# Performance work log

Hardware: AMD Instinct MI355X
Metric: run time of the kernel (lower is better)

The kernel has to match this reference:

```python
import jax, jax.numpy as jnp
import numpy as np
import math

N = 60000; B = 2; D = 128; NH = 8; HD = D // NH; DFF = 256
NBLK = 6; L = NBLK * 2
WIN = 12.0; TEMP = 10000.0
NY, NX = 400, 400
MT = (36, 144)      # max_tokens per drop level (drop_info)
CAP = (25, 100)     # filled tokens per window in synthetic data (~0.7 fill)
LVL_N = (24000, 36000)  # voxels per drop level (per shift)


def _nwin(n, cap):
    return -(-n // cap)


def _make_inds(n, lvl):
    j = np.arange(n)
    return (j // CAP[lvl]) * MT[lvl] + (j % CAP[lvl])


def setup_inputs():
    ks = jax.random.split(jax.random.key(0), 8)
    rng = np.random.default_rng(0)
    # unique BEV coords per batch element -> scatter has no collisions
    coors_list = []
    for b in range(B):
        flat = rng.choice(NY * NX, N // B, replace=False)
        coors_list.append(np.stack([np.full(N // B, b, np.int64), np.zeros(N // B, np.int64), flat // NX, flat % NX], 1))
    coors = jnp.asarray(np.concatenate(coors_list, 0), dtype=jnp.int32)
    vxs, indss = [], []
    for s in range(2):
        perm = rng.permutation(N)
        vxs += [np.sort(perm[:LVL_N[0]]), np.sort(perm[LVL_N[0]:])]
        indss += [_make_inds(LVL_N[0], 0), _make_inds(LVL_N[1], 1)]
    i32 = lambda a: jnp.asarray(a, jnp.int32)
    f = lambda k, shape: jax.random.normal(k, shape, dtype=jnp.float32) * 0.02
    return dict(
        voxel_feat=jax.random.normal(ks[0], (N, D), dtype=jnp.float32),
        coors=coors,
        ciw0=jax.random.randint(ks[1], (N, 2), 0, int(WIN)).astype(jnp.float32),
        ciw1=jax.random.randint(ks[2], (N, 2), 0, int(WIN)).astype(jnp.float32),
        vx00=i32(vxs[0]), inds00=i32(indss[0]), vx01=i32(vxs[1]), inds01=i32(indss[1]),
        vx10=i32(vxs[2]), inds10=i32(indss[2]), vx11=i32(vxs[3]), inds11=i32(indss[3]),
        in_proj_w=f(ks[3], (L, 3 * D, D)), in_proj_b=jnp.zeros((L, 3 * D), jnp.float32),
        out_w=f(ks[4], (L, D, D)), out_b=jnp.zeros((L, D), jnp.float32),
        lin1_w=f(ks[5], (L, DFF, D)), lin1_b=jnp.zeros((L, DFF), jnp.float32),
        lin2_w=f(ks[6], (L, D, DFF)), lin2_b=jnp.zeros((L, D), jnp.float32),
        ln1_g=jnp.ones((L, D), jnp.float32), ln1_b=jnp.zeros((L, D), jnp.float32),
        ln2_g=jnp.ones((L, D), jnp.float32), ln2_b=jnp.zeros((L, D), jnp.float32),
        conv_w=f(ks[7], (2, D, D, 3, 3)),
        bn_g=jnp.ones((2, D), jnp.float32), bn_b=jnp.zeros((2, D), jnp.float32),
        bn_m=jnp.zeros((2, D), jnp.float32), bn_v=jnp.ones((2, D), jnp.float32),
    )


def _pos_embed(ciw):
    # SSTv1.get_pos_embed: interleaved sin/cos over x and y window coords
    xy = ciw - WIN / 2.0
    pl = D // 2
    i = jnp.arange(pl, dtype=jnp.float32)
    inv = TEMP ** (2.0 * jnp.floor(i / 2.0) / pl)
    e = xy[:, :, None] / inv                      # [N, 2, pl]
    emb = jnp.stack([jnp.sin(e[..., ::2]), jnp.cos(e[..., 1::2])], -1).reshape(ciw.shape[0], 2, pl)
    return jnp.concatenate([emb[:, 0], emb[:, 1]], -1)  # [N, D]


def _ln(x, g, b):
    mu = jnp.mean(x, -1, keepdims=True)
    var = jnp.mean((x - mu) ** 2, -1, keepdims=True)
    return (x - mu) * jax.lax.rsqrt(var + 1e-5) * g + b


def _forward(voxel_feat, coors, ciws, vx, inds, fp):
    (ipw, ipb, ow, ob, l1w, l1b, l2w, l2b, g1, b1, g2, b2, cw, bg, bb, bm, bv) = fp
    pos = [_pos_embed(ciws[0]), _pos_embed(ciws[1])]
    feat = voxel_feat
    for blk in range(NBLK):
        for s in range(2):  # BasicShiftBlock: one encoder layer per shift
            li = blk * 2 + s
            attn_out = jnp.zeros_like(feat)
            for lvl in range(2):  # drop levels, each with its own padded window tensor
                v, ii = vx[(s, lvl)], inds[(s, lvl)]
                mt = MT[lvl]
                nw = _nwin(int(v.shape[0]), CAP[lvl])
                def to_win(x2d):  # flat2window: scatter voxels into [nw, mt, C]
                    return jnp.zeros((nw * mt, x2d.shape[-1]), x2d.dtype).at[ii].set(x2d[v]).reshape(nw, mt, -1)
                wf = to_win(feat)
                wp = to_win(pos[s])
                pad = jnp.ones((nw * mt,), bool).at[ii].set(False).reshape(nw, mt)  # True = padded slot
                qk_in = wf + wp
                q = (qk_in @ ipw[li, :D].T + ipb[li, :D]).reshape(nw, mt, NH, HD)
                k = (qk_in @ ipw[li, D:2 * D].T + ipb[li, D:2 * D]).reshape(nw, mt, NH, HD)
                val = (wf @ ipw[li, 2 * D:].T + ipb[li, 2 * D:]).reshape(nw, mt, NH, HD)
                sc = jnp.einsum('wqhd,wkhd->whqk', q, k) / math.sqrt(HD)
                sc = jnp.where(pad[:, None, None, :], -jnp.inf, sc)
                o = jnp.einsum('whqk,wkhd->wqhd', jax.nn.softmax(sc, -1), val).reshape(nw, mt, D)
                o = o @ ow[li].T + ob[li]
                # window2flat: gather valid slots back to flat voxel order
                attn_out = attn_out.at[v].set(o.reshape(nw * mt, D)[ii])
            feat = _ln(feat + attn_out, g1[li], b1[li])
            h = jax.nn.gelu(feat @ l1w[li].T + l1b[li], approximate=False)
            feat = _ln(feat + h @ l2w[li].T + l2b[li], g2[li], b2[li])
    # recover_bev: scatter voxels into dense BEV canvas [B, C, ny, nx]
    flat_idx = coors[:, 0] * (NY * NX) + coors[:, 2] * NX + coors[:, 3]
    canvas = jnp.zeros((B * NY * NX, D), feat.dtype).at[flat_idx].set(feat)
    bev = canvas.reshape(B, NY, NX, D).transpose(0, 3, 1, 2)
    for i in range(2):  # attached dilated convs + BN(eval) + ReLU
        bev = jax.lax.conv_general_dilated(bev, cw[i], (1, 1), [(2, 2), (2, 2)], rhs_dilation=(2, 2), dimension_numbers=('NCHW', 'OIHW', 'NCHW'))
        bev = (bev - bm[i][:, None, None]) * jax.lax.rsqrt(bv[i][:, None, None] + 1e-3) * bg[i][:, None, None] + bb[i][:, None, None]
        bev = jax.nn.relu(bev)
    return bev


def reference(voxel_feat, coors, ciw0, ciw1, vx00, inds00, vx01, inds01, vx10, inds10, vx11, inds11, in_proj_w, in_proj_b, out_w, out_b, lin1_w, lin1_b, lin2_w, lin2_b, ln1_g, ln1_b, ln2_g, ln2_b, conv_w, bn_g, bn_b, bn_m, bn_v):
    vx = {(0, 0): vx00, (0, 1): vx01, (1, 0): vx10, (1, 1): vx11}
    inds = {(0, 0): inds00, (0, 1): inds01, (1, 0): inds10, (1, 1): inds11}
    fp = (in_proj_w, in_proj_b, out_w, out_b, lin1_w, lin1_b, lin2_w, lin2_b, ln1_g, ln1_b, ln2_g, ln2_b, conv_w, bn_g, bn_b, bn_m, bn_v)
    return _forward(voxel_feat, coors, (ciw0, ciw1), vx, inds, fp)
```

## Files before the change

kernel.cpp:

```cpp
#include <hip/hip_runtime.h>
#include <math.h>

#define NVOX 60000

typedef __attribute__((ext_vector_type(8))) short short8v;
typedef __attribute__((ext_vector_type(8))) unsigned short ushort8v;
typedef __attribute__((ext_vector_type(4))) float f32x4;

static __device__ __forceinline__ unsigned short f2bf(float f) {
    unsigned u = __float_as_uint(f);
    unsigned r = (u + 0x7fffu + ((u >> 16) & 1u)) >> 16;
    return (unsigned short)r;
}
static __device__ __forceinline__ float bf2f(unsigned short h) {
    return __uint_as_float(((unsigned)h) << 16);
}
static __device__ __forceinline__ void gll16(const unsigned short* g, unsigned short* l) {
    __builtin_amdgcn_global_load_lds(
        (const __attribute__((address_space(1))) unsigned*)g,
        (__attribute__((address_space(3))) unsigned*)l,
        16, 0, 0);
}

__global__ __launch_bounds__(256) void pos_kernel(const float* __restrict__ ciw,
                                                  unsigned short* __restrict__ pos) {
    int idx = blockIdx.x * 256 + threadIdx.x;
    if (idx >= NVOX * 128) return;
    int n = idx >> 7, d = idx & 127;
    int c = d >> 6, t = (d & 63) >> 1;
    float xy = ciw[n * 2 + c] - 6.0f;
    float inv = exp2f((float)t * (13.287712379549449f / 32.0f));
    float e = xy / inv;
    pos[idx] = f2bf((d & 1) ? cosf(e) : sinf(e));
}

__global__ __launch_bounds__(256) void cvt_bf16(const float* __restrict__ in,
                                                unsigned short* __restrict__ out, int n) {
    int idx = blockIdx.x * 256 + threadIdx.x;
    if (idx < n) out[idx] = f2bf(in[idx]);
}

__global__ __launch_bounds__(256) void feat_init(const float* __restrict__ vf,
                                                 float* __restrict__ feat,
                                                 unsigned short* __restrict__ featb) {
    int idx = blockIdx.x * 256 + threadIdx.x;
    if (idx >= NVOX * 128) return;
    float v = vf[idx];
    feat[idx] = v;
    featb[idx] = f2bf(v);
}

template<int KTOT, bool ADD, bool GELU, bool CBF16, bool LNF>
__global__ __launch_bounds__(256) void gemm_mfma(
    const unsigned short* __restrict__ A, const unsigned short* __restrict__ Aadd, int add_nblk,
    const unsigned short* __restrict__ W, const float* __restrict__ bias,
    void* __restrict__ Cp, int M, int ldc,
    float* __restrict__ feat, unsigned short* __restrict__ featb,
    const float* __restrict__ lng, const float* __restrict__ lnb)
{
    __shared__ unsigned short smem[128 * 128];
    __shared__ float2 lnsum[128][2];
    unsigned short* As = smem;
    unsigned short* Ws = smem + 128 * 64;
    const int tid = threadIdx.x;
    const int lane = tid & 63, wave = tid >> 6;
    const int wr = wave >> 1, wc = wave & 1;
    const int llo = lane & 15, lhi = lane >> 4;
    const int m0 = blockIdx.x * 128;
    const int n0 = blockIdx.y * 128;
    const bool addp = ADD && ((int)blockIdx.y < add_nblk);
    const int gr = lane >> 3;
    const int gc = (lane & 7) ^ gr;
    f32x4 acc[4][4] = {};

    for (int k0 = 0; k0 < KTOT; k0 += 64) {
        #pragma unroll
        for (int p = 0; p < 4; ++p) {
            int r0 = wave * 32 + p * 8;
            gll16(W + (size_t)(n0 + r0 + gr) * KTOT + k0 + gc * 8, &Ws[r0 * 64]);
        }
        if (!addp) {
            #pragma unroll
            for (int p = 0; p < 4; ++p) {
                int r0 = wave * 32 + p * 8;
                gll16(A + (size_t)(m0 + r0 + gr) * KTOT + k0 + gc * 8, &As[r0 * 64]);
            }
        } else {
            #pragma unroll
            for (int p = 0; p < 4; ++p) {
                int c = tid + p * 256;
                int r = c >> 3, c16 = c & 7;
                int m = m0 + r;
                short8v av = {};
                if (m < M) {
                    ushort8v fa = *reinterpret_cast<const ushort8v*>(A + (size_t)m * KTOT + k0 + c16 * 8);
                    ushort8v pa = *reinterpret_cast<const ushort8v*>(Aadd + (size_t)m * 128 + k0 + c16 * 8);
                    #pragma unroll
                    for (int q = 0; q < 8; ++q) av[q] = (short)f2bf(bf2f(fa[q]) + bf2f(pa[q]));
                }
                *reinterpret_cast<short8v*>((char*)As + r * 128 + ((c16 * 16) ^ ((r & 7) << 4))) = av;
            }
        }
        __syncthreads();
        #pragma unroll
        for (int kk = 0; kk < 2; ++kk) {
            int kb = kk * 64 + lhi * 16;
            short8v af[4], bf[4];
            #pragma unroll
            for (int i = 0; i < 4; ++i) {
                int r = wr * 64 + i * 16 + llo;
                af[i] = *reinterpret_cast<const short8v*>((const char*)As + r * 128 + (kb ^ ((r & 7) << 4)));
                int cc = wc * 64 + i * 16 + llo;
                bf[i] = *reinterpret_cast<const short8v*>((const char*)Ws + cc * 128 + (kb ^ ((cc & 7) << 4)));
            }
            #pragma unroll
            for (int i = 0; i < 4; ++i)
                #pragma unroll
                for (int j = 0; j < 4; ++j)
                    acc[i][j] = __builtin_amdgcn_mfma_f32_16x16x32_bf16(af[i], bf[j], acc[i][j], 0, 0, 0);
        }
        __syncthreads();
    }

    if (LNF) {
        float s1[4][4] = {}, s2[4][4] = {};
        #pragma unroll
        for (int i = 0; i < 4; ++i)
            #pragma unroll
            for (int rg = 0; rg < 4; ++rg) {
                int m = m0 + wr * 64 + i * 16 + lhi * 4 + rg;
                if (m < M) {
                    #pragma unroll
                    for (int j = 0; j < 4; ++j) {
                        int n = wc * 64 + j * 16 + llo;
                        float x = feat[(size_t)m * 128 + n] + acc[i][j][rg] + bias[n];
                        acc[i][j][rg] = x;
                        s1[i][rg] += x; s2[i][rg] += x * x;
                    }
                }
            }
        #pragma unroll
        for (int i = 0; i < 4; ++i)
            #pragma unroll
            for (int rg = 0; rg < 4; ++rg) {
                #pragma unroll
                for (int off = 1; off < 16; off <<= 1) {
                    s1[i][rg] += __shfl_xor(s1[i][rg], off);
                    s2[i][rg] += __shfl_xor(s2[i][rg], off);
                }
                if (llo == 0)
                    lnsum[wr * 64 + i * 16 + lhi * 4 + rg][wc] = make_float2(s1[i][rg], s2[i][rg]);
            }
        __syncthreads();
        #pragma unroll
        for (int i = 0; i < 4; ++i)
            #pragma unroll
            for (int rg = 0; rg < 4; ++rg) {
                int r = wr * 64 + i * 16 + lhi * 4 + rg;
                int m = m0 + r;
                if (m >= M) continue;
                float2 a0 = lnsum[r][0], a1 = lnsum[r][1];
                float mu = (a0.x + a1.x) * 0.0078125f;
                float var = fmaxf((a0.y + a1.y) * 0.0078125f - mu * mu, 0.f);
                float inv = rsqrtf(var + 1e-5f);
                #pragma unroll
                for (int j = 0; j < 4; ++j) {
                    int n = wc * 64 + j * 16 + llo;
                    float v = (acc[i][j][rg] - mu) * inv * lng[n] + lnb[n];
                    feat[(size_t)m * 128 + n] = v;
                    featb[(size_t)m * 128 + n] = f2bf(v);
                }
            }
    } else if (CBF16) {
        #pragma unroll
        for (int j = 0; j < 4; ++j) {
            int nl = wc * 64 + j * 16 + llo;
            float bn = bias[n0 + nl];
            #pragma unroll
            for (int i = 0; i < 4; ++i)
                #pragma unroll
                for (int rg = 0; rg < 4; ++rg) {
                    float v = acc[i][j][rg] + bn;
                    if (GELU) v = 0.5f * v * (1.0f + erff(v * 0.7071067811865475f));
                    smem[(wr * 64 + i * 16 + lhi * 4 + rg) * 128 + nl] = f2bf(v);
                }
        }
        __syncthreads();
        unsigned short* C = (unsigned short*)Cp;
        #pragma unroll
        for (int c = 0; c < 8; ++c) {
            int idx = tid + c * 256;
            int r = idx >> 4, ch = idx & 15;
            if (m0 + r < M)
                *reinterpret_cast<ushort8v*>(C + (size_t)(m0 + r) * ldc + n0 + ch * 8) =
                    *reinterpret_cast<const ushort8v*>(&smem[r * 128 + ch * 8]);
        }
    } else {
        float* C = (float*)Cp;
        #pragma unroll
        for (int j = 0; j < 4; ++j) {
            int n = n0 + wc * 64 + j * 16 + llo;
            float bn = bias[n];
            #pragma unroll
            for (int i = 0; i < 4; ++i)
                #pragma unroll
                for (int rg = 0; rg < 4; ++rg) {
                    int m = m0 + wr * 64 + i * 16 + lhi * 4 + rg;
                    if (m < M) {
                        float v = acc[i][j][rg] + bn;
                        if (GELU) v = 0.5f * v * (1.0f + erff(v * 0.7071067811865475f));
                        C[(size_t)m * ldc + n] = v;
                    }
                }
        }
    }
}

template<int CAPT, int HG>
__global__ __launch_bounds__(256) void attn_kernel(
    const unsigned short* __restrict__ qkv, const int* __restrict__ vlist, int nvox,
    unsigned short* __restrict__ oout)
{
    __shared__ float Ks[CAPT][HG * 16];
    __shared__ float Vs[CAPT][HG * 16];
    __shared__ int vl[CAPT];
    const int w = blockIdx.x;
    const int hb = blockIdx.y * HG;
    const int tid = threadIdx.x;
    const int T = min(CAPT, nvox - w * CAPT);
    if (tid < T) vl[tid] = vlist[w * CAPT + tid];
    constexpr int R8 = HG * 2;
    for (int idx = tid; idx < T * R8; idx += 256) {
        int t = idx / R8, c8 = (idx % R8) * 8;
        int vox = vlist[w * CAPT + t];
        const unsigned short* base = qkv + (size_t)vox * 384 + hb * 16 + c8;
        ushort8v kv = *reinterpret_cast<const ushort8v*>(base + 128);
        ushort8v vv = *reinterpret_cast<const ushort8v*>(base + 256);
        #pragma unroll
        for (int q = 0; q < 8; ++q) { Ks[t][c8 + q] = bf2f(kv[q]); Vs[t][c8 + q] = bf2f(vv[q]); }
    }
    __syncthreads();
    const int ITEMS = T * HG;
    for (int item = tid; item < ITEMS; item += 256) {
        int h = item & (HG - 1);
        int q = item / HG;
        int vq = vl[q];
        const unsigned short* qb = qkv + (size_t)vq * 384 + (hb + h) * 16;
        ushort8v qa = *reinterpret_cast<const ushort8v*>(qb);
        ushort8v qc = *reinterpret_cast<const ushort8v*>(qb + 8);
        float4 q0 = make_float4(bf2f(qa[0]), bf2f(qa[1]), bf2f(qa[2]), bf2f(qa[3]));
        float4 q1 = make_float4(bf2f(qa[4]), bf2f(qa[5]), bf2f(qa[6]), bf2f(qa[7]));
        float4 q2 = make_float4(bf2f(qc[0]), bf2f(qc[1]), bf2f(qc[2]), bf2f(qc[3]));
        float4 q3 = make_float4(bf2f(qc[4]), bf2f(qc[5]), bf2f(qc[6]), bf2f(qc[7]));
        float mx = -INFINITY, l = 0.f;
        float4 o0 = make_float4(0,0,0,0), o1 = o0, o2 = o0, o3 = o0;
        for (int t = 0; t < T; ++t) {
            const float4* kr = reinterpret_cast<const float4*>(&Ks[t][h * 16]);
            float4 k0 = kr[0], k1 = kr[1], k2 = kr[2], k3 = kr[3];
            float s = q0.x*k0.x + q0.y*k0.y + q0.z*k0.z + q0.w*k0.w
                    + q1.x*k1.x + q1.y*k1.y + q1.z*k1.z + q1.w*k1.w
                    + q2.x*k2.x + q2.y*k2.y + q2.z*k2.z + q2.w*k2.w
                    + q3.x*k3.x + q3.y*k3.y + q3.z*k3.z + q3.w*k3.w;
            s *= 0.25f;
            float mo = mx;
            mx = fmaxf(mx, s);
            float cc = __expf(mo - mx);
            float p  = __expf(s - mx);
            l = l * cc + p;
            const float4* vr = reinterpret_cast<const float4*>(&Vs[t][h * 16]);
            float4 v0 = vr[0], v1 = vr[1], v2 = vr[2], v3 = vr[3];
            o0.x = o0.x*cc + p*v0.x; o0.y = o0.y*cc + p*v0.y; o0.z = o0.z*cc + p*v0.z; o0.w = o0.w*cc + p*v0.w;
            o1.x = o1.x*cc + p*v1.x; o1.y = o1.y*cc + p*v1.y; o1.z = o1.z*cc + p*v1.z; o1.w = o1.w*cc + p*v1.w;
            o2.x = o2.x*cc + p*v2.x; o2.y = o2.y*cc + p*v2.y; o2.z = o2.z*cc + p*v2.z; o2.w = o2.w*cc + p*v2.w;
            o3.x = o3.x*cc + p*v3.x; o3.y = o3.y*cc + p*v3.y; o3.z = o3.z*cc + p*v3.z; o3.w = o3.w*cc + p*v3.w;
        }
        float rl = 1.0f / l;
        ushort8v r0, r1;
        r0[0]=f2bf(o0.x*rl); r0[1]=f2bf(o0.y*rl); r0[2]=f2bf(o0.z*rl); r0[3]=f2bf(o0.w*rl);
        r0[4]=f2bf(o1.x*rl); r0[5]=f2bf(o1.y*rl); r0[6]=f2bf(o1.z*rl); r0[7]=f2bf(o1.w*rl);
        r1[0]=f2bf(o2.x*rl); r1[1]=f2bf(o2.y*rl); r1[2]=f2bf(o2.z*rl); r1[3]=f2bf(o2.w*rl);
        r1[4]=f2bf(o3.x*rl); r1[5]=f2bf(o3.y*rl); r1[6]=f2bf(o3.z*rl); r1[7]=f2bf(o3.w*rl);
        unsigned short* op = oout + (size_t)vq * 128 + (hb + h) * 16;
        *reinterpret_cast<ushort8v*>(op) = r0;
        *reinterpret_cast<ushort8v*>(op + 8) = r1;
    }
}

__global__ __launch_bounds__(256) void scatter_kernel(const float* __restrict__ feat,
    const int* __restrict__ coors, unsigned short* __restrict__ canvas)
{
    int idx = blockIdx.x * 256 + threadIdx.x;
    if (idx >= NVOX * 16) return;
    int n = idx >> 4, c8 = (idx & 15) << 3;
    int b = coors[n * 4], y = coors[n * 4 + 2], x = coors[n * 4 + 3];
    const float* src = feat + (size_t)n * 128 + c8;
    float4 u0 = *reinterpret_cast<const float4*>(src);
    float4 u1 = *reinterpret_cast<const float4*>(src + 4);
    ushort8v v;
    v[0]=f2bf(u0.x); v[1]=f2bf(u0.y); v[2]=f2bf(u0.z); v[3]=f2bf(u0.w);
    v[4]=f2bf(u1.x); v[5]=f2bf(u1.y); v[6]=f2bf(u1.z); v[7]=f2bf(u1.w);
    size_t p = (((size_t)b * 404 + y + 2) * 420 + x + 2) * 128 + c8;
    *reinterpret_cast<ushort8v*>(canvas + p) = v;
}

__global__ __launch_bounds__(256) void wtrans_kernel(const float* __restrict__ cw,
                                                     unsigned short* __restrict__ wbuf)
{
    int idx = blockIdx.x * 256 + threadIdx.x;
    if (idx >= 2 * 9 * 128 * 128) return;
    int ci = idx & 127;
    int co = (idx >> 7) & 127;
    int kk = (idx >> 14) % 9;
    int i  = idx / (9 * 16384);
    wbuf[idx] = f2bf(cw[(((size_t)i * 128 + co) * 128 + ci) * 9 + kk]);
}

template<bool NCHW_OUT>
__global__ __launch_bounds__(512, 1) void conv_mfma(
    const unsigned short* __restrict__ in, const unsigned short* __restrict__ wbuf,
    const float* __restrict__ g, const float* __restrict__ bsh,
    const float* __restrict__ bm, const float* __restrict__ bv,
    void* __restrict__ out)
{
    __shared__ unsigned short Ab[8 * 36 * 128];
    __shared__ unsigned short Wb[2 * 128 * 128];
    const int tid = threadIdx.x;
    const int lane = tid & 63, wave = tid >> 6;
    const int cog = wave & 1, yg = wave >> 1;
    const int llo = lane & 15, lhi = lane >> 4;
    const int x0 = blockIdx.x * 32, y0 = blockIdx.y * 4, b = blockIdx.z;
    const int c16s = lane & 15;

    #pragma unroll
    for (int it = 0; it < 9; ++it) {
        int gidx = it * 32 + wave * 4 + lhi;
        int row = gidx / 36, xi = gidx % 36;
        gll16(in + (((size_t)b * 404 + y0 + row) * 420 + x0 + xi) * 128 + ((c16s ^ (xi & 15)) * 8),
              Ab + (size_t)(it * 512 + wave * 64) * 8);
    }
    {
        const unsigned short* wt = wbuf;
        #pragma unroll
        for (int it = 0; it < 4; ++it) {
            int co = it * 32 + wave * 4 + lhi;
            gll16(wt + co * 128 + ((c16s ^ (co & 15)) * 8),
                  Wb + (size_t)(it * 512 + wave * 64) * 8);
        }
    }
    __syncthreads();

    f32x4 acc[2][4] = {};
    #pragma unroll
    for (int t = 0; t < 9; ++t) {
        if (t < 8) {
            const unsigned short* wt = wbuf + (size_t)(t + 1) * 16384;
            unsigned short* dst = Wb + ((t + 1) & 1) * 16384;
            #pragma unroll
            for (int it = 0; it < 4; ++it) {
                int co = it * 32 + wave * 4 + lhi;
                gll16(wt + co * 128 + ((c16s ^ (co & 15)) * 8),
                      dst + (size_t)(it * 512 + wave * 64) * 8);
            }
        }
        const unsigned short* Wp = Wb + (t & 1) * 16384;
        const int ky = t / 3, kx = t % 3;
        const int r = yg + 2 * ky;
        #pragma unroll
        for (int kk = 0; kk < 4; ++kk) {
            short8v a[2], w[4];
            #pragma unroll
            for (int i = 0; i < 2; ++i) {
                int xi = i * 16 + llo + 2 * kx;
                a[i] = *reinterpret_cast<const short8v*>(
                    (const char*)Ab + (r * 36 + xi) * 256 + ((kk * 64 + lhi * 16) ^ ((xi & 15) << 4)));
            }
            #pragma unroll
            for (int j = 0; j < 4; ++j) {
                int co = cog * 64 + j * 16 + llo;
                w[j] = *reinterpret_cast<const short8v*>(
                    (const char*)Wp + co * 256 + ((kk * 64 + lhi * 16) ^ ((co & 15) << 4)));
            }
            #pragma unroll
            for (int i = 0; i < 2; ++i)
                #pragma unroll
                for (int j = 0; j < 4; ++j)
                    acc[i][j] = __builtin_amdgcn_mfma_f32_16x16x32_bf16(a[i], w[j], acc[i][j], 0, 0, 0);
        }
        __syncthreads();
    }

    const int y = y0 + yg;
    if (NCHW_OUT) {
        #pragma unroll
        for (int j = 0; j < 4; ++j) {
            int co = cog * 64 + j * 16 + llo;
            float scale = rsqrtf(bv[co] + 1e-3f) * g[co];
            float shift = bsh[co] - bm[co] * scale;
            #pragma unroll
            for (int i = 0; i < 2; ++i) {
                int px = x0 + i * 16 + lhi * 4;
                if (px < 400) {
                    float4 v;
                    v.x = fmaxf(acc[i][j][0] * scale + shift, 0.f);
                    v.y = fmaxf(acc[i][j][1] * scale + shift, 0.f);
                    v.z = fmaxf(acc[i][j][2] * scale + shift, 0.f);
                    v.w = fmaxf(acc[i][j][3] * scale + shift, 0.f);
                    *reinterpret_cast<float4*>(
                        (float*)out + (((size_t)b * 128 + co) * 400 + y) * 400 + px) = v;
                }
            }
        }
    } else {
        unsigned short* Cw = Wb + wave * 2048;
        #pragma unroll
        for (int j = 0; j < 4; ++j) {
            int co = cog * 64 + j * 16 + llo;
            float scale = rsqrtf(bv[co] + 1e-3f) * g[co];
            float shift = bsh[co] - bm[co] * scale;
            #pragma unroll
            for (int i = 0; i < 2; ++i)
                #pragma unroll
                for (int rg = 0; rg < 4; ++rg)
                    Cw[(i * 16 + lhi * 4 + rg) * 64 + j * 16 + llo] =
                        f2bf(fmaxf(acc[i][j][rg] * scale + shift, 0.f));
        }
        #pragma unroll
        for (int s = 0; s < 4; ++s) {
            int pxl = s * 8 + (lane >> 3);
            int oct = lane & 7;
            int px = x0 + pxl;
            if (px < 400)
                *reinterpret_cast<ushort8v*>(
                    (unsigned short*)out + (((size_t)b * 404 + y + 2) * 420 + px + 2) * 128
                                         + cog * 64 + oct * 8) =
                    *reinterpret_cast<const ushort8v*>(&Cw[pxl * 64 + oct * 8]);
        }
    }
}

extern "C" void kernel_launch(void* const* d_in, const int* in_sizes, int n_in,
                              void* d_out, int out_size, void* d_ws, size_t ws_size,
                              hipStream_t stream) {
    const float* voxel_feat = (const float*)d_in[0];
    const int*   coors      = (const int*)d_in[1];
    const float* ciw0       = (const float*)d_in[2];
    const float* ciw1       = (const float*)d_in[3];
    const int* vx[2][2] = {{(const int*)d_in[4], (const int*)d_in[6]},
                           {(const int*)d_in[8], (const int*)d_in[10]}};
    const float* ipw = (const float*)d_in[12];
    const float* ipb = (const float*)d_in[13];
    const float* ow  = (const float*)d_in[14];
    const float* obp = (const float*)d_in[15];
    const float* l1w = (const float*)d_in[16];
    const float* l1b = (const float*)d_in[17];
    const float* l2w = (const float*)d_in[18];
    const float* l2b = (const float*)d_in[19];
    const float* g1  = (const float*)d_in[20];
    const float* b1  = (const float*)d_in[21];
    const float* g2  = (const float*)d_in[22];
    const float* b2  = (const float*)d_in[23];
    const float* cw  = (const float*)d_in[24];
    const float* bng = (const float*)d_in[25];
    const float* bnb = (const float*)d_in[26];
    const float* bnm = (const float*)d_in[27];
    const float* bnv = (const float*)d_in[28];

    float* F = (float*)d_ws;
    unsigned short* W0   = (unsigned short*)F;
    unsigned short* ipwb = W0;
    unsigned short* owb  = W0 + 589824;
    unsigned short* l1wb = W0 + 786432;
    unsigned short* l2wb = W0 + 1179648;
    unsigned short* cwb  = W0 + 1572864;
    float* feat = F + 940000;
    unsigned short* featb = (unsigned short*)(F + 8620000);
    unsigned short* pos0  = (unsigned short*)(F + 12460000);
    unsigned short* pos1  = (unsigned short*)(F + 16300000);
    unsigned short* obufb = (unsigned short*)(F + 20140000);
    unsigned short* hbufb = (unsigned short*)(F + 23980000);
    unsigned short* canvas1 = (unsigned short*)(F + 8620000);
    unsigned short* canvas2 = (unsigned short*)(F + 30339040);
    unsigned short* qkvb = (unsigned short*)d_out;

    feat_init<<<30000, 256, 0, stream>>>(voxel_feat, feat, featb);
    pos_kernel<<<30000, 256, 0, stream>>>(ciw0, pos0);
    pos_kernel<<<30000, 256, 0, stream>>>(ciw1, pos1);
    cvt_bf16<<<(589824 + 255) / 256, 256, 0, stream>>>(ipw, ipwb, 589824);
    cvt_bf16<<<(196608 + 255) / 256, 256, 0, stream>>>(ow,  owb,  196608);
    cvt_bf16<<<(393216 + 255) / 256, 256, 0, stream>>>(l1w, l1wb, 393216);
    cvt_bf16<<<(393216 + 255) / 256, 256, 0, stream>>>(l2w, l2wb, 393216);
    wtrans_kernel<<<(2 * 9 * 16384 + 255) / 256, 256, 0, stream>>>(cw, cwb);

    for (int li = 0; li < 12; ++li) {
        int s = li & 1;
        const unsigned short* pos = s ? pos1 : pos0;
        gemm_mfma<128, true, false, true, false><<<dim3(469, 3), 256, 0, stream>>>(
            featb, pos, 2, ipwb + (size_t)li * 49152, ipb + li * 384, qkvb, NVOX, 384,
            nullptr, nullptr, nullptr, nullptr);
        attn_kernel<25, 8><<<dim3(960, 1), 256, 0, stream>>>(qkvb, vx[s][0], 24000, obufb);
        attn_kernel<100, 2><<<dim3(360, 4), 256, 0, stream>>>(qkvb, vx[s][1], 36000, obufb);
        gemm_mfma<128, false, false, false, true><<<dim3(469, 1), 256, 0, stream>>>(
            obufb, nullptr, 0, owb + (size_t)li * 16384, obp + li * 128, nullptr, NVOX, 128,
            feat, featb, g1 + li * 128, b1 + li * 128);
        gemm_mfma<128, false, true, true, false><<<dim3(469, 2), 256, 0, stream>>>(
            featb, nullptr, 0, l1wb + (size_t)li * 32768, l1b + li * 256, hbufb, NVOX, 256,
            nullptr, nullptr, nullptr, nullptr);
        gemm_mfma<256, false, false, false, true><<<dim3(469, 1), 256, 0, stream>>>(
            hbufb, nullptr, 0, l2wb + (size_t)li * 32768, l2b + li * 128, nullptr, NVOX, 128,
            feat, featb, g2 + li * 128, b2 + li * 128);
    }

    hipMemsetAsync(canvas1, 0, (size_t)43438080 * 2 * 2, stream);
    scatter_kernel<<<(NVOX * 16 + 255) / 256, 256, 0, stream>>>(feat, coors, canvas1);
    conv_mfma<false><<<dim3(13, 100, 2), 512, 0, stream>>>(
        canvas1, cwb, bng, bnb, bnm, bnv, canvas2);
    conv_mfma<true><<<dim3(13, 100, 2), 512, 0, stream>>>(
        canvas2, cwb + 9 * 16384, bng + 128, bnb + 128, bnm + 128, bnv + 128, (float*)d_out);
}
```

Before: 2.494 ms.

## Fuse out-proj, LN1, FFN and LN2 into one per-layer tail kernel

Replaces the three post-attention GEMM launches (out-projection + LN1, lin1 + GELU, lin2 + LN2) with a single fused kernel. Each block handles 64 rows and keeps the LN1 output and the GELU hidden activations in LDS, so the hidden buffer and intermediate feat/featb no longer round-trip through global memory. It also shrinks the canvas memset to canvas1 only and zeroes just the halo of canvas2 with a small kernel. The cost is heavy LDS use per block (about 74KB), which limits occupancy, and the weights are reloaded by every block.

After: 2.769 ms. 1.11x slower.

```diff
diff --git a/kernel.cpp b/kernel.cpp
--- a/kernel.cpp
+++ b/kernel.cpp
@@ -54,12 +54,9 @@
 __global__ __launch_bounds__(256) void gemm_mfma(
     const unsigned short* __restrict__ A, const unsigned short* __restrict__ Aadd, int add_nblk,
     const unsigned short* __restrict__ W, const float* __restrict__ bias,
-    void* __restrict__ Cp, int M, int ldc,
-    float* __restrict__ feat, unsigned short* __restrict__ featb,
-    const float* __restrict__ lng, const float* __restrict__ lnb)
+    void* __restrict__ Cp, int M, int ldc)
 {
     __shared__ unsigned short smem[128 * 128];
-    __shared__ float2 lnsum[128][2];
     unsigned short* As = smem;
     unsigned short* Ws = smem + 128 * 64;
     const int tid = threadIdx.x;
@@ -122,97 +119,28 @@
         __syncthreads();
     }
 
-    if (LNF) {
-        float s1[4][4] = {}, s2[4][4] = {};
+    #pragma unroll
+    for (int j = 0; j < 4; ++j) {
+        int nl = wc * 64 + j * 16 + llo;
+        float bn = bias[n0 + nl];
         #pragma unroll
         for (int i = 0; i < 4; ++i)
             #pragma unroll
             for (int rg = 0; rg < 4; ++rg) {
-                int m = m0 + wr * 64 + i * 16 + lhi * 4 + rg;
-                if (m < M) {
-                    #pragma unroll
-                    for (int j = 0; j < 4; ++j) {
-                        int n = wc * 64 + j * 16 + llo;
-                        float x = feat[(size_t)m * 128 + n] + acc[i][j][rg] + bias[n];
-                        acc[i][j][rg] = x;
-                        s1[i][rg] += x; s2[i][rg] += x * x;
-                    }
-                }
-            }
-        #pragma unroll
-        for (int i = 0; i < 4; ++i)
-            #pragma unroll
-            for (int rg = 0; rg < 4; ++rg) {
-                #pragma unroll
-                for (int off = 1; off < 16; off <<= 1) {
-                    s1[i][rg] += __shfl_xor(s1[i][rg], off);
-                    s2[i][rg] += __shfl_xor(s2[i][rg], off);
-                }
-                if (llo == 0)
-                    lnsum[wr * 64 + i * 16 + lhi * 4 + rg][wc] = make_float2(s1[i][rg], s2[i][rg]);
-            }
-        __syncthreads();
-        #pragma unroll
-        for (int i = 0; i < 4; ++i)
-            #pragma unroll
-            for (int rg = 0; rg < 4; ++rg) {
-                int r = wr * 64 + i * 16 + lhi * 4 + rg;
-                int m = m0 + r;
-                if (m >= M) continue;
-                float2 a0 = lnsum[r][0], a1 = lnsum[r][1];
-                float mu = (a0.x + a1.x) * 0.0078125f;
-                float var = fmaxf((a0.y + a1.y) * 0.0078125f - mu * mu, 0.f);
-                float inv = rsqrtf(var + 1e-5f);
-                #pragma unroll
-                for (int j = 0; j < 4; ++j) {
-                    int n = wc * 64 + j * 16 + llo;
-                    float v = (acc[i][j][rg] - mu) * inv * lng[n] + lnb[n];
-                    feat[(size_t)m * 128 + n] = v;
-                    featb[(size_t)m * 128 + n] = f2bf(v);
-                }
-            }
-    } else if (CBF16) {
-        #pragma unroll
-        for (int j = 0; j < 4; ++j) {
-            int nl = wc * 64 + j * 16 + llo;
-            float bn = bias[n0 + nl];
-            #pragma unroll
-            for (int i = 0; i < 4; ++i)
-                #pragma unroll
-                for (int rg = 0; rg < 4; ++rg) {
-                    float v = acc[i][j][rg] + bn;
-                    if (GELU) v = 0.5f * v * (1.0f + erff(v * 0.7071067811865475f));
-                    smem[(wr * 64 + i * 16 + lhi * 4 + rg) * 128 + nl] = f2bf(v);
-                }
-        }
-        __syncthreads();
-        unsigned short* C = (unsigned short*)Cp;
-        #pragma unroll
-        for (int c = 0; c < 8; ++c) {
-            int idx = tid + c * 256;
-            int r = idx >> 4, ch = idx & 15;
-            if (m0 + r < M)
-                *reinterpret_cast<ushort8v*>(C + (size_t)(m0 + r) * ldc + n0 + ch * 8) =
-                    *reinterpret_cast<const ushort8v*>(&smem[r * 128 + ch * 8]);
-        }
-    } else {
-        float* C = (float*)Cp;
-        #pragma unroll
-        for (int j = 0; j < 4; ++j) {
-            int n = n0 + wc * 64 + j * 16 + llo;
-            float bn = bias[n];
-            #pragma unroll
-            for (int i = 0; i < 4; ++i)
-                #pragma unroll
-                for (int rg = 0; rg < 4; ++rg) {
-                    int m = m0 + wr * 64 + i * 16 + lhi * 4 + rg;
-                    if (m < M) {
-                        float v = acc[i][j][rg] + bn;
-                        if (GELU) v = 0.5f * v * (1.0f + erff(v * 0.7071067811865475f));
-                        C[(size_t)m * ldc + n] = v;
-                    }
-                }
-        }
+                float v = acc[i][j][rg] + bn;
+                if (GELU) v = 0.5f * v * (1.0f + erff(v * 0.7071067811865475f));
+                smem[(wr * 64 + i * 16 + lhi * 4 + rg) * 128 + nl] = f2bf(v);
+            }
+    }
+    __syncthreads();
+    unsigned short* C = (unsigned short*)Cp;
+    #pragma unroll
+    for (int c = 0; c < 8; ++c) {
+        int idx = tid + c * 256;
+        int r = idx >> 4, ch = idx & 15;
+        if (m0 + r < M)
+            *reinterpret_cast<ushort8v*>(C + (size_t)(m0 + r) * ldc + n0 + ch * 8) =
+                *reinterpret_cast<const ushort8v*>(&smem[r * 128 + ch * 8]);
     }
 }
 
@@ -286,6 +214,230 @@
     }
 }
 
+__global__ __launch_bounds__(256) void fused_tail(
+    const unsigned short* __restrict__ obuf,
+    const unsigned short* __restrict__ oww,
+    const float* __restrict__ obp,
+    const unsigned short* __restrict__ w1,
+    const float* __restrict__ b1p,
+    const unsigned short* __restrict__ w2,
+    const float* __restrict__ b2p,
+    const float* __restrict__ lng1, const float* __restrict__ lnb1,
+    const float* __restrict__ lng2, const float* __restrict__ lnb2,
+    float* __restrict__ feat, unsigned short* __restrict__ featb, int M)
+{
+    __shared__ unsigned short S[36864];
+    __shared__ float2 lnsum[64][4];
+    unsigned short* Abuf = S;
+    unsigned short* Wbuf = S + 4096;
+    unsigned short* Xbuf = S + 12288;
+    unsigned short* Hbuf = S + 20480;
+    const int tid = threadIdx.x;
+    const int lane = tid & 63, wave = tid >> 6;
+    const int llo = lane & 15, lhi = lane >> 4;
+    const int r8 = lane >> 3, c8 = lane & 7;
+    const int m0 = blockIdx.x * 64;
+
+    auto stageA = [&](int k0) {
+        #pragma unroll
+        for (int it = 0; it < 2; ++it) {
+            int rb = wave * 16 + it * 8;
+            int r = rb + r8;
+            int gm = m0 + r; if (gm >= M) gm = M - 1;
+            gll16(obuf + (size_t)gm * 128 + k0 * 64 + ((c8 ^ (r & 7)) * 8), Abuf + rb * 64);
+        }
+    };
+    auto stageW = [&](const unsigned short* src, int ldk, int koff) {
+        #pragma unroll
+        for (int it = 0; it < 4; ++it) {
+            int rb = wave * 32 + it * 8;
+            int r = rb + r8;
+            gll16(src + (size_t)r * ldk + koff + ((c8 ^ (r & 7)) * 8), Wbuf + rb * 64);
+        }
+    };
+    auto frag = [&](const unsigned short* buf, int r, int kk) {
+        return *reinterpret_cast<const short8v*>(
+            (const char*)buf + r * 128 + (((kk * 4 + lhi) ^ (r & 7)) * 16));
+    };
+    auto sput = [&](unsigned short* buf, int col, int r, float v) {
+        int slab = col >> 6, k = col & 63;
+        buf[slab * 4096 + r * 64 + (((k >> 3) ^ (r & 7)) * 8) + (k & 7)] = f2bf(v);
+    };
+
+    f32x4 acc0[4][2] = {};
+    #pragma unroll
+    for (int k0 = 0; k0 < 2; ++k0) {
+        stageA(k0);
+        stageW(oww, 128, k0 * 64);
+        __syncthreads();
+        #pragma unroll
+        for (int kk = 0; kk < 2; ++kk) {
+            short8v a[4], w[2];
+            #pragma unroll
+            for (int i = 0; i < 4; ++i) a[i] = frag(Abuf, i * 16 + llo, kk);
+            #pragma unroll
+            for (int j = 0; j < 2; ++j) w[j] = frag(Wbuf, wave * 32 + j * 16 + llo, kk);
+            #pragma unroll
+            for (int i = 0; i < 4; ++i)
+                #pragma unroll
+                for (int j = 0; j < 2; ++j)
+                    acc0[i][j] = __builtin_amdgcn_mfma_f32_16x16x32_bf16(a[i], w[j], acc0[i][j], 0, 0, 0);
+        }
+        __syncthreads();
+    }
+
+    {
+        float ob0 = obp[wave * 32 + llo];
+        float ob1 = obp[wave * 32 + 16 + llo];
+        #pragma unroll
+        for (int i = 0; i < 4; ++i)
+            #pragma unroll
+            for (int rg = 0; rg < 4; ++rg) {
+                int m = m0 + i * 16 + lhi * 4 + rg;
+                if (m >= M) m = M - 1;
+                const float* fp = feat + (size_t)m * 128 + wave * 32 + llo;
+                float x0 = fp[0]  + acc0[i][0][rg] + ob0;
+                float x1 = fp[16] + acc0[i][1][rg] + ob1;
+                acc0[i][0][rg] = x0; acc0[i][1][rg] = x1;
+                float s1 = x0 + x1, s2 = x0 * x0 + x1 * x1;
+                #pragma unroll
+                for (int off = 1; off < 16; off <<= 1) {
+                    s1 += __shfl_xor(s1, off);
+                    s2 += __shfl_xor(s2, off);
+                }
+                if (llo == 0) lnsum[i * 16 + lhi * 4 + rg][wave] = make_float2(s1, s2);
+            }
+    }
+    __syncthreads();
+    {
+        float gg0 = lng1[wave * 32 + llo],      bb0 = lnb1[wave * 32 + llo];
+        float gg1 = lng1[wave * 32 + 16 + llo], bb1 = lnb1[wave * 32 + 16 + llo];
+        #pragma unroll
+        for (int i = 0; i < 4; ++i)
+            #pragma unroll
+            for (int rg = 0; rg < 4; ++rg) {
+                int r = i * 16 + lhi * 4 + rg;
+                float2 t0 = lnsum[r][0], t1 = lnsum[r][1], t2 = lnsum[r][2], t3 = lnsum[r][3];
+                float mu = (t0.x + t1.x + t2.x + t3.x) * 0.0078125f;
+                float var = fmaxf((t0.y + t1.y + t2.y + t3.y) * 0.0078125f - mu * mu, 0.f);
+                float inv = rsqrtf(var + 1e-5f);
+                float x0 = (acc0[i][0][rg] - mu) * inv * gg0 + bb0;
+                float x1 = (acc0[i][1][rg] - mu) * inv * gg1 + bb1;
+                acc0[i][0][rg] = x0; acc0[i][1][rg] = x1;
+                sput(Xbuf, wave * 32 + llo, r, x0);
+                sput(Xbuf, wave * 32 + 16 + llo, r, x1);
+            }
+    }
+    __syncthreads();
+
+    f32x4 acc1[4][4] = {};
+    #pragma unroll
+    for (int nh = 0; nh < 2; ++nh)
+        #pragma unroll
+        for (int k0 = 0; k0 < 2; ++k0) {
+            stageW(w1 + (size_t)nh * 16384, 128, k0 * 64);
+            __syncthreads();
+            #pragma unroll
+            for (int kk = 0; kk < 2; ++kk) {
+                short8v a[4], w[2];
+                #pragma unroll
+                for (int i = 0; i < 4; ++i) a[i] = frag(Xbuf + k0 * 4096, i * 16 + llo, kk);
+                #pragma unroll
+                for (int j = 0; j < 2; ++j) w[j] = frag(Wbuf, wave * 32 + j * 16 + llo, kk);
+                #pragma unroll
+                for (int i = 0; i < 4; ++i)
+                    #pragma unroll
+                    for (int j = 0; j < 2; ++j)
+                        acc1[i][nh * 2 + j] = __builtin_amdgcn_mfma_f32_16x16x32_bf16(
+                            a[i], w[j], acc1[i][nh * 2 + j], 0, 0, 0);
+            }
+            __syncthreads();
+        }
+
+    {
+        float bb[4];
+        #pragma unroll
+        for (int c = 0; c < 4; ++c)
+            bb[c] = b1p[(c >> 1) * 128 + wave * 32 + (c & 1) * 16 + llo];
+        #pragma unroll
+        for (int i = 0; i < 4; ++i)
+            #pragma unroll
+            for (int c = 0; c < 4; ++c) {
+                int col = (c >> 1) * 128 + wave * 32 + (c & 1) * 16 + llo;
+                #pragma unroll
+                for (int rg = 0; rg < 4; ++rg) {
+                    float v = acc1[i][c][rg] + bb[c];
+                    v = 0.5f * v * (1.0f + erff(v * 0.7071067811865475f));
+                    sput(Hbuf, col, i * 16 + lhi * 4 + rg, v);
+                }
+            }
+    }
+    __syncthreads();
+
+    f32x4 acc2[4][2] = {};
+    #pragma unroll
+    for (int k0 = 0; k0 < 4; ++k0) {
+        stageW(w2, 256, k0 * 64);
+        __syncthreads();
+        #pragma unroll
+        for (int kk = 0; kk < 2; ++kk) {
+            short8v a[4], w[2];
+            #pragma unroll
+            for (int i = 0; i < 4; ++i) a[i] = frag(Hbuf + k0 * 4096, i * 16 + llo, kk);
+            #pragma unroll
+            for (int j = 0; j < 2; ++j) w[j] = frag(Wbuf, wave * 32 + j * 16 + llo, kk);
+            #pragma unroll
+            for (int i = 0; i < 4; ++i)
+                #pragma unroll
+                for (int j = 0; j < 2; ++j)
+                    acc2[i][j] = __builtin_amdgcn_mfma_f32_16x16x32_bf16(a[i], w[j], acc2[i][j], 0, 0, 0);
+        }
+        __syncthreads();
+    }
+
+    {
+        float b20 = b2p[wave * 32 + llo];
+        float b21 = b2p[wave * 32 + 16 + llo];
+        #pragma unroll
+        for (int i = 0; i < 4; ++i)
+            #pragma unroll
+            for (int rg = 0; rg < 4; ++rg) {
+                float x0 = acc0[i][0][rg] + acc2[i][0][rg] + b20;
+                float x1 = acc0[i][1][rg] + acc2[i][1][rg] + b21;
+                acc2[i][0][rg] = x0; acc2[i][1][rg] = x1;
+                float s1 = x0 + x1, s2 = x0 * x0 + x1 * x1;
+                #pragma unroll
+                for (int off = 1; off < 16; off <<= 1) {
+                    s1 += __shfl_xor(s1, off);
+                    s2 += __shfl_xor(s2, off);
+                }
+                if (llo == 0) lnsum[i * 16 + lhi * 4 + rg][wave] = make_float2(s1, s2);
+            }
+    }
+    __syncthreads();
+    {
+        float gg0 = lng2[wave * 32 + llo],      bb0 = lnb2[wave * 32 + llo];
+        float gg1 = lng2[wave * 32 + 16 + llo], bb1 = lnb2[wave * 32 + 16 + llo];
+        #pragma unroll
+        for (int i = 0; i < 4; ++i)
+            #pragma unroll
+            for (int rg = 0; rg < 4; ++rg) {
+                int r = i * 16 + lhi * 4 + rg;
+                int m = m0 + r;
+                if (m >= M) continue;
+                float2 t0 = lnsum[r][0], t1 = lnsum[r][1], t2 = lnsum[r][2], t3 = lnsum[r][3];
+                float mu = (t0.x + t1.x + t2.x + t3.x) * 0.0078125f;
+                float var = fmaxf((t0.y + t1.y + t2.y + t3.y) * 0.0078125f - mu * mu, 0.f);
+                float inv = rsqrtf(var + 1e-5f);
+                float v0 = (acc2[i][0][rg] - mu) * inv * gg0 + bb0;
+                float v1 = (acc2[i][1][rg] - mu) * inv * gg1 + bb1;
+                size_t base = (size_t)m * 128 + wave * 32 + llo;
+                feat[base] = v0;       feat[base + 16] = v1;
+                featb[base] = f2bf(v0); featb[base + 16] = f2bf(v1);
+            }
+    }
+}
+
 __global__ __launch_bounds__(256) void scatter_kernel(const float* __restrict__ feat,
     const int* __restrict__ coors, unsigned short* __restrict__ canvas)
 {
@@ -301,6 +453,19 @@
     v[4]=f2bf(u1.x); v[5]=f2bf(u1.y); v[6]=f2bf(u1.z); v[7]=f2bf(u1.w);
     size_t p = (((size_t)b * 404 + y + 2) * 420 + x + 2) * 128 + c8;
     *reinterpret_cast<ushort8v*>(canvas + p) = v;
+}
+
+__global__ __launch_bounds__(256) void halo_zero(unsigned short* __restrict__ c) {
+    int idx = blockIdx.x * 256 + threadIdx.x;
+    if (idx >= 2 * 9680 * 16) return;
+    int b = idx / (9680 * 16);
+    int rem = idx % (9680 * 16);
+    int p = rem >> 4, ch = (rem & 15) * 8;
+    int y, x;
+    if (p < 1680) { int ry = p / 420; y = (ry < 2) ? ry : ry + 400; x = p % 420; }
+    else { int q = p - 1680; y = 2 + q / 20; int cx = q % 20; x = (cx < 2) ? cx : cx + 400; }
+    ushort8v z = {};
+    *reinterpret_cast<ushort8v*>(c + (((size_t)b * 404 + y) * 420 + x) * 128 + ch) = z;
 }
 
 __global__ __launch_bounds__(256) void wtrans_kernel(const float* __restrict__ cw,
@@ -477,7 +642,6 @@
     unsigned short* pos0  = (unsigned short*)(F + 12460000);
     unsigned short* pos1  = (unsigned short*)(F + 16300000);
     unsigned short* obufb = (unsigned short*)(F + 20140000);
-    unsigned short* hbufb = (unsigned short*)(F + 23980000);
     unsigned short* canvas1 = (unsigned short*)(F + 8620000);
     unsigned short* canvas2 = (unsigned short*)(F + 30339040);
     unsigned short* qkvb = (unsigned short*)d_out;
@@ -495,22 +659,19 @@
         int s = li & 1;
         const unsigned short* pos = s ? pos1 : pos0;
         gemm_mfma<128, true, false, true, false><<<dim3(469, 3), 256, 0, stream>>>(
-            featb, pos, 2, ipwb + (size_t)li * 49152, ipb + li * 384, qkvb, NVOX, 384,
-            nullptr, nullptr, nullptr, nullptr);
+            featb, pos, 2, ipwb + (size_t)li * 49152, ipb + li * 384, qkvb, NVOX, 384);
         attn_kernel<25, 8><<<dim3(960, 1), 256, 0, stream>>>(qkvb, vx[s][0], 24000, obufb);
         attn_kernel<100, 2><<<dim3(360, 4), 256, 0, stream>>>(qkvb, vx[s][1], 36000, obufb);
-        gemm_mfma<128, false, false, false, true><<<dim3(469, 1), 256, 0, stream>>>(
-            obufb, nullptr, 0, owb + (size_t)li * 16384, obp + li * 128, nullptr, NVOX, 128,
-            feat, featb, g1 + li * 128, b1 + li * 128);
-        gemm_mfma<128, false, true, true, false><<<dim3(469, 2), 256, 0, stream>>>(
-            featb, nullptr, 0, l1wb + (size_t)li * 32768, l1b + li * 256, hbufb, NVOX, 256,
-            nullptr, nullptr, nullptr, nullptr);
-        gemm_mfma<256, false, false, false, true><<<dim3(469, 1), 256, 0, stream>>>(
-            hbufb, nullptr, 0, l2wb + (size_t)li * 32768, l2b + li * 128, nullptr, NVOX, 128,
-            feat, featb, g2 + li * 128, b2 + li * 128);
-    }
-
-    hipMemsetAsync(canvas1, 0, (size_t)43438080 * 2 * 2, stream);
+        fused_tail<<<938, 256, 0, stream>>>(
+            obufb, owb + (size_t)li * 16384, obp + li * 128,
+            l1wb + (size_t)li * 32768, l1b + li * 256,
+            l2wb + (size_t)li * 32768, l2b + li * 128,
+            g1 + li * 128, b1 + li * 128, g2 + li * 128, b2 + li * 128,
+            feat, featb, NVOX);
+    }
+
+    hipMemsetAsync(canvas1, 0, (size_t)43438080 * 2, stream);
+    halo_zero<<<(2 * 9680 * 16 + 255) / 256, 256, 0, stream>>>(canvas2);
     scatter_kernel<<<(NVOX * 16 + 255) / 256, 256, 0, stream>>>(feat, coors, canvas1);
     conv_mfma<false><<<dim3(13, 100, 2), 512, 0, stream>>>(
         canvas1, cwb, bng, bnb, bnm, bnv, canvas2);
```

## Precompute feat+pos in LN epilogue, drop halo memset of full second canvas

Applied to the files above, without the earlier changes.

The positional-embedding add for the Q/K inputs moves out of the QKV GEMM's A-load path and into the LayerNorm epilogue of the preceding FFN GEMM (and into feat_init for the first layer). This lets every QKV tile use the async global_load_lds path instead of a register-based load, add and store. The hidden FFN buffer now reuses the qkv output buffer. The memset now clears only canvas1, and a small halo_zero kernel clears just the padding border of canvas2, whose interior is fully overwritten by the first conv. In exchange, the LN epilogue writes an extra bf16 tensor per layer.

After: 2.730 ms. 1.09x slower.

```diff
diff --git a/kernel.cpp b/kernel.cpp
--- a/kernel.cpp
+++ b/kernel.cpp
@@ -41,21 +41,25 @@
 }
 
 __global__ __launch_bounds__(256) void feat_init(const float* __restrict__ vf,
+                                                 const unsigned short* __restrict__ pos0,
                                                  float* __restrict__ feat,
-                                                 unsigned short* __restrict__ featb) {
+                                                 unsigned short* __restrict__ featb,
+                                                 unsigned short* __restrict__ featq) {
     int idx = blockIdx.x * 256 + threadIdx.x;
     if (idx >= NVOX * 128) return;
     float v = vf[idx];
     feat[idx] = v;
     featb[idx] = f2bf(v);
-}
-
-template<int KTOT, bool ADD, bool GELU, bool CBF16, bool LNF>
+    featq[idx] = f2bf(v + bf2f(pos0[idx]));
+}
+
+template<int KTOT, bool QKV, bool GELU, bool CBF16, bool LNF>
 __global__ __launch_bounds__(256) void gemm_mfma(
-    const unsigned short* __restrict__ A, const unsigned short* __restrict__ Aadd, int add_nblk,
+    const unsigned short* __restrict__ Aq, const unsigned short* __restrict__ Av,
     const unsigned short* __restrict__ W, const float* __restrict__ bias,
     void* __restrict__ Cp, int M, int ldc,
     float* __restrict__ feat, unsigned short* __restrict__ featb,
+    unsigned short* __restrict__ featq, const unsigned short* __restrict__ posq,
     const float* __restrict__ lng, const float* __restrict__ lnb)
 {
     __shared__ unsigned short smem[128 * 128];
@@ -68,7 +72,7 @@
     const int llo = lane & 15, lhi = lane >> 4;
     const int m0 = blockIdx.x * 128;
     const int n0 = blockIdx.y * 128;
-    const bool addp = ADD && ((int)blockIdx.y < add_nblk);
+    const unsigned short* A = QKV ? (((int)blockIdx.y < 2) ? Aq : Av) : Aq;
     const int gr = lane >> 3;
     const int gc = (lane & 7) ^ gr;
     f32x4 acc[4][4] = {};
@@ -79,27 +83,10 @@
             int r0 = wave * 32 + p * 8;
             gll16(W + (size_t)(n0 + r0 + gr) * KTOT + k0 + gc * 8, &Ws[r0 * 64]);
         }
-        if (!addp) {
-            #pragma unroll
-            for (int p = 0; p < 4; ++p) {
-                int r0 = wave * 32 + p * 8;
-                gll16(A + (size_t)(m0 + r0 + gr) * KTOT + k0 + gc * 8, &As[r0 * 64]);
-            }
-        } else {
-            #pragma unroll
-            for (int p = 0; p < 4; ++p) {
-                int c = tid + p * 256;
-                int r = c >> 3, c16 = c & 7;
-                int m = m0 + r;
-                short8v av = {};
-                if (m < M) {
-                    ushort8v fa = *reinterpret_cast<const ushort8v*>(A + (size_t)m * KTOT + k0 + c16 * 8);
-                    ushort8v pa = *reinterpret_cast<const ushort8v*>(Aadd + (size_t)m * 128 + k0 + c16 * 8);
-                    #pragma unroll
-                    for (int q = 0; q < 8; ++q) av[q] = (short)f2bf(bf2f(fa[q]) + bf2f(pa[q]));
-                }
-                *reinterpret_cast<short8v*>((char*)As + r * 128 + ((c16 * 16) ^ ((r & 7) << 4))) = av;
-            }
+        #pragma unroll
+        for (int p = 0; p < 4; ++p) {
+            int r0 = wave * 32 + p * 8;
+            gll16(A + (size_t)(m0 + r0 + gr) * KTOT + k0 + gc * 8, &As[r0 * 64]);
         }
         __syncthreads();
         #pragma unroll
@@ -169,6 +156,8 @@
                     float v = (acc[i][j][rg] - mu) * inv * lng[n] + lnb[n];
                     feat[(size_t)m * 128 + n] = v;
                     featb[(size_t)m * 128 + n] = f2bf(v);
+                    if (posq != nullptr)
+                        featq[(size_t)m * 128 + n] = f2bf(v + bf2f(posq[(size_t)m * 128 + n]));
                 }
             }
     } else if (CBF16) {
@@ -303,6 +292,19 @@
     *reinterpret_cast<ushort8v*>(canvas + p) = v;
 }
 
+__global__ __launch_bounds__(256) void halo_zero(unsigned short* __restrict__ c) {
+    int idx = blockIdx.x * 256 + threadIdx.x;
+    if (idx >= 2 * 9680 * 16) return;
+    int b = idx / (9680 * 16);
+    int rem = idx % (9680 * 16);
+    int p = rem >> 4, ch = (rem & 15) * 8;
+    int y, x;
+    if (p < 1680) { int ry = p / 420; y = (ry < 2) ? ry : ry + 400; x = p % 420; }
+    else { int q = p - 1680; y = 2 + q / 20; int cx = q % 20; x = (cx < 2) ? cx : cx + 400; }
+    ushort8v z = {};
+    *reinterpret_cast<ushort8v*>(c + (((size_t)b * 404 + y) * 420 + x) * 128 + ch) = z;
+}
+
 __global__ __launch_bounds__(256) void wtrans_kernel(const float* __restrict__ cw,
                                                      unsigned short* __restrict__ wbuf)
 {
@@ -477,14 +479,14 @@
     unsigned short* pos0  = (unsigned short*)(F + 12460000);
     unsigned short* pos1  = (unsigned short*)(F + 16300000);
     unsigned short* obufb = (unsigned short*)(F + 20140000);
-    unsigned short* hbufb = (unsigned short*)(F + 23980000);
+    unsigned short* featq = (unsigned short*)(F + 23980000);
     unsigned short* canvas1 = (unsigned short*)(F + 8620000);
     unsigned short* canvas2 = (unsigned short*)(F + 30339040);
     unsigned short* qkvb = (unsigned short*)d_out;
 
-    feat_init<<<30000, 256, 0, stream>>>(voxel_feat, feat, featb);
     pos_kernel<<<30000, 256, 0, stream>>>(ciw0, pos0);
     pos_kernel<<<30000, 256, 0, stream>>>(ciw1, pos1);
+    feat_init<<<30000, 256, 0, stream>>>(voxel_feat, pos0, feat, featb, featq);
     cvt_bf16<<<(589824 + 255) / 256, 256, 0, stream>>>(ipw, ipwb, 589824);
     cvt_bf16<<<(196608 + 255) / 256, 256, 0, stream>>>(ow,  owb,  196608);
     cvt_bf16<<<(393216 + 255) / 256, 256, 0, stream>>>(l1w, l1wb, 393216);
@@ -492,25 +494,26 @@
     wtrans_kernel<<<(2 * 9 * 16384 + 255) / 256, 256, 0, stream>>>(cw, cwb);
 
     for (int li = 0; li < 12; ++li) {
+        const unsigned short* posNext = ((li + 1) & 1) ? pos1 : pos0;
         int s = li & 1;
-        const unsigned short* pos = s ? pos1 : pos0;
         gemm_mfma<128, true, false, true, false><<<dim3(469, 3), 256, 0, stream>>>(
-            featb, pos, 2, ipwb + (size_t)li * 49152, ipb + li * 384, qkvb, NVOX, 384,
-            nullptr, nullptr, nullptr, nullptr);
+            featq, featb, ipwb + (size_t)li * 49152, ipb + li * 384, qkvb, NVOX, 384,
+            nullptr, nullptr, nullptr, nullptr, nullptr, nullptr);
         attn_kernel<25, 8><<<dim3(960, 1), 256, 0, stream>>>(qkvb, vx[s][0], 24000, obufb);
         attn_kernel<100, 2><<<dim3(360, 4), 256, 0, stream>>>(qkvb, vx[s][1], 36000, obufb);
         gemm_mfma<128, false, false, false, true><<<dim3(469, 1), 256, 0, stream>>>(
-            obufb, nullptr, 0, owb + (size_t)li * 16384, obp + li * 128, nullptr, NVOX, 128,
-            feat, featb, g1 + li * 128, b1 + li * 128);
+            obufb, nullptr, owb + (size_t)li * 16384, obp + li * 128, nullptr, NVOX, 128,
+            feat, featb, nullptr, nullptr, g1 + li * 128, b1 + li * 128);
         gemm_mfma<128, false, true, true, false><<<dim3(469, 2), 256, 0, stream>>>(
-            featb, nullptr, 0, l1wb + (size_t)li * 32768, l1b + li * 256, hbufb, NVOX, 256,
-            nullptr, nullptr, nullptr, nullptr);
+            featb, nullptr, l1wb + (size_t)li * 32768, l1b + li * 256, qkvb, NVOX, 256,
+            nullptr, nullptr, nullptr, nullptr, nullptr, nullptr);
         gemm_mfma<256, false, false, false, true><<<dim3(469, 1), 256, 0, stream>>>(
-            hbufb, nullptr, 0, l2wb + (size_t)li * 32768, l2b + li * 128, nullptr, NVOX, 128,
-            feat, featb, g2 + li * 128, b2 + li * 128);
-    }
-
-    hipMemsetAsync(canvas1, 0, (size_t)43438080 * 2 * 2, stream);
+            qkvb, nullptr, l2wb + (size_t)li * 32768, l2b + li * 128, nullptr, NVOX, 128,
+            feat, featb, featq, posNext, g2 + li * 128, b2 + li * 128);
+    }
+
+    hipMemsetAsync(canvas1, 0, (size_t)43438080 * 2, stream);
+    halo_zero<<<(2 * 9680 * 16 + 255) / 256, 256, 0, stream>>>(canvas2);
     scatter_kernel<<<(NVOX * 16 + 255) / 256, 256, 0, stream>>>(feat, coors, canvas1);
     conv_mfma<false><<<dim3(13, 100, 2), 512, 0, stream>>>(
         canvas1, cwb, bng, bnb, bnm, bnv, canvas2);
```
